# Kernel tuning notes

Measured on AMD Instinct MI355X. Metric: run time of the kernel, lower is better.

The kernel has to match this reference:

```python
import jax, jax.numpy as jnp
import numpy as np

B, S, D, H = 4, 2048, 1024, 16
DH = D // H


def setup_inputs() -> dict:
    key = jax.random.key(0)
    k0, k1, k2, k3 = jax.random.split(key, 4)
    x = jax.random.normal(k0, (B, S, D), dtype=jnp.float32)
    k = jax.random.normal(k1, (B, H, S, DH), dtype=jnp.float32)
    v = jax.random.normal(k2, (B, H, S, DH), dtype=jnp.float32)
    # nn.Linear(d, d, bias=False) weight: [out, in]; scaled like torch default init
    Wq = jax.random.normal(k3, (D, D), dtype=jnp.float32) * (1.0 / np.sqrt(D))
    return {"x": x, "k": k, "v": v, "Wq": Wq}


def reference(x, k, v, Wq):
    Bx, Sx, d = x.shape
    h, dh = k.shape[1], k.shape[3]
    rd = jnp.sqrt(jnp.float32(d))  # NOTE: module scales by sqrt(d), not sqrt(d_head)
    # q projection: y = x @ Wq.T  -> [B,S,d] -> [B,h,S,dh]
    q = (x @ Wq.T).reshape(Bx, Sx, h, dh).transpose(0, 2, 1, 3)
    # scores [B,h,S,S]
    a = jnp.einsum('bhqd,bhkd->bhqk', q, k) / rd
    causal = jnp.triu(jnp.ones((Sx, Sx), dtype=bool), k=1)
    a = jnp.where(causal, -jnp.inf, a)
    p = jax.nn.softmax(a, axis=-1)
    o = jnp.einsum('bhqk,bhkd->bhqd', p, v)  # [B,h,S,dh]
    o = o.transpose(0, 2, 1, 3).reshape(Bx, Sx, d)
    return x + o
```

## Files before the change

### kernel.cpp

```cpp
#include <hip/hip_runtime.h>
#include <hip/hip_bf16.h>

typedef __attribute__((ext_vector_type(4))) float f32x4;
typedef __attribute__((ext_vector_type(8))) short bf16x8;
typedef __attribute__((ext_vector_type(4))) unsigned short u16x4;

#define MFMA16(a, b, c) __builtin_amdgcn_mfma_f32_16x16x32_bf16((a), (b), (c), 0, 0, 0)

static __device__ __forceinline__ unsigned short f2bf(float f) {
    unsigned u = __float_as_uint(f);
    u += 0x7FFFu + ((u >> 16) & 1u);
    return (unsigned short)(u >> 16);
}
static __device__ __forceinline__ uint2 pack4_rhu(float4 v) {
    unsigned a = __float_as_uint(v.x) + 0x8000u;
    unsigned b = __float_as_uint(v.y) + 0x8000u;
    unsigned c = __float_as_uint(v.z) + 0x8000u;
    unsigned d = __float_as_uint(v.w) + 0x8000u;
    uint2 r;
    r.x = __builtin_amdgcn_perm(b, a, 0x07060302u);
    r.y = __builtin_amdgcn_perm(d, c, 0x07060302u);
    return r;
}
static __device__ __forceinline__ float exp2_fast(float x) {
#if __has_builtin(__builtin_amdgcn_exp2f)
    return __builtin_amdgcn_exp2f(x);
#else
    return exp2f(x);
#endif
}

#define QSCALE 0.04508422002778011f

__global__ __launch_bounds__(256) void qproj_kernel(const float* __restrict__ x,
                                                    const float* __restrict__ wq,
                                                    unsigned short* __restrict__ qout) {
    __shared__ __align__(16) unsigned short As[2][128][40];
    __shared__ __align__(16) unsigned short Bs[2][128][40];
    const int m0 = blockIdx.x * 128;
    const int n0 = blockIdx.y * 128;
    const int tid = threadIdx.x;
    const int wave = tid >> 6, lane = tid & 63;
    const int lg = lane >> 4, lc = lane & 15;
    const int wm = wave >> 1, wn = wave & 1;

    f32x4 acc[4][4];
#pragma unroll
    for (int i = 0; i < 4; ++i)
#pragma unroll
        for (int j = 0; j < 4; ++j) acc[i][j] = (f32x4){0.f, 0.f, 0.f, 0.f};

    float4 ax[4], bx[4];
#pragma unroll
    for (int i = 0; i < 4; ++i) {
        int c = tid + i * 256;
        int row = c >> 3, kc = (c & 7) * 4;
        ax[i] = *(const float4*)(x  + (size_t)(m0 + row) * 1024 + kc);
        bx[i] = *(const float4*)(wq + (size_t)(n0 + row) * 1024 + kc);
    }
#pragma unroll
    for (int i = 0; i < 4; ++i) {
        int c = tid + i * 256;
        int row = c >> 3, kc = (c & 7) * 4;
        *(uint2*)&As[0][row][kc] = pack4_rhu(ax[i]);
        *(uint2*)&Bs[0][row][kc] = pack4_rhu(bx[i]);
    }

    int cur = 0;
    for (int ki = 0; ki < 32; ++ki) {
        __syncthreads();
        const bool havenext = (ki + 1 < 32);
        if (havenext) {
            int ks = (ki + 1) * 32;
#pragma unroll
            for (int i = 0; i < 4; ++i) {
                int c = tid + i * 256;
                int row = c >> 3, kc = (c & 7) * 4;
                ax[i] = *(const float4*)(x  + (size_t)(m0 + row) * 1024 + ks + kc);
                bx[i] = *(const float4*)(wq + (size_t)(n0 + row) * 1024 + ks + kc);
            }
        }
        bf16x8 af[4], bfr[4];
#pragma unroll
        for (int i = 0; i < 4; ++i) {
            af[i]  = *(const bf16x8*)&As[cur][wm * 64 + i * 16 + lc][lg * 8];
            bfr[i] = *(const bf16x8*)&Bs[cur][wn * 64 + i * 16 + lc][lg * 8];
        }
        __builtin_amdgcn_s_setprio(1);
#pragma unroll
        for (int mi = 0; mi < 4; ++mi)
#pragma unroll
            for (int ni = 0; ni < 4; ++ni)
                acc[mi][ni] = MFMA16(af[mi], bfr[ni], acc[mi][ni]);
        __builtin_amdgcn_s_setprio(0);
        if (havenext) {
#pragma unroll
            for (int i = 0; i < 4; ++i) {
                int c = tid + i * 256;
                int row = c >> 3, kc = (c & 7) * 4;
                *(uint2*)&As[cur ^ 1][row][kc] = pack4_rhu(ax[i]);
                *(uint2*)&Bs[cur ^ 1][row][kc] = pack4_rhu(bx[i]);
            }
        }
        cur ^= 1;
    }
#pragma unroll
    for (int mi = 0; mi < 4; ++mi)
#pragma unroll
        for (int ni = 0; ni < 4; ++ni)
#pragma unroll
            for (int r = 0; r < 4; ++r) {
                int m = m0 + wm * 64 + mi * 16 + lg * 4 + r;
                int n = n0 + wn * 64 + ni * 16 + lc;
                int b = m >> 11, s = m & 2047;
                int h = n >> 6, dh = n & 63;
                qout[(((size_t)b * 16 + h) * 2048 + s) * 64 + dh] = f2bf(acc[mi][ni][r] * QSCALE);
            }
}

__global__ __launch_bounds__(256) void convtrans_kernel(const float* __restrict__ kin,
                                                        const float* __restrict__ vin,
                                                        unsigned short* __restrict__ kb,
                                                        unsigned short* __restrict__ vt) {
    __shared__ float buf[64][65];
    const int bid = blockIdx.x;
    const int tid = threadIdx.x;
    if (bid < 8192) {
        int i = bid * 256 + tid;
        float4 v = ((const float4*)kin)[i];
        u16x4 o = { f2bf(v.x), f2bf(v.y), f2bf(v.z), f2bf(v.w) };
        ((u16x4*)kb)[i] = o;
    } else {
        const int idx = bid - 8192;
        const int s0 = (idx & 31) * 64;
        const int bh = idx >> 5;
#pragma unroll
        for (int i = 0; i < 4; ++i) {
            int c = tid + i * 256;
            int s = c >> 4, dc = (c & 15) * 4;
            float4 val = *(const float4*)(vin + ((size_t)bh * 2048 + s0 + s) * 64 + dc);
            buf[s][dc] = val.x; buf[s][dc + 1] = val.y; buf[s][dc + 2] = val.z; buf[s][dc + 3] = val.w;
        }
        __syncthreads();
#pragma unroll
        for (int i = 0; i < 4; ++i) {
            int c = tid + i * 256;
            int dh = c >> 4, sc = (c & 15) * 4;
            u16x4 o = { f2bf(buf[sc][dh]), f2bf(buf[sc + 1][dh]), f2bf(buf[sc + 2][dh]), f2bf(buf[sc + 3][dh]) };
            *(u16x4*)(vt + ((size_t)bh * 64 + dh) * 2048 + s0 + sc) = o;
        }
    }
}

__global__ __launch_bounds__(256, 3) void attn_kernel(const unsigned short* __restrict__ qg,
                                                      const unsigned short* __restrict__ kg,
                                                      const unsigned short* __restrict__ vtg,
                                                      const float* __restrict__ x,
                                                      float* __restrict__ outp) {
    __shared__ __align__(16) unsigned short Ks[2][64][64];
    __shared__ __align__(16) unsigned short VTs[2][64][64];
    __shared__ __align__(16) unsigned short Ps[4][32][72];

    const int bh = blockIdx.x;
    const int qb = 15 - blockIdx.y;
    const int b = bh >> 4, h = bh & 15;
    const int tid = threadIdx.x;
    const int wave = tid >> 6, lane = tid & 63;
    const int lg = lane >> 4, lc = lane & 15;
    const int lc7 = lc & 7;
    const int qw0 = qb * 128 + wave * 32;
    const int nkv = 2 * qb + 2;

    const int r0  = tid >> 3;
    const int c16 = tid & 7;
    const int swz = (c16 ^ (r0 & 7)) * 8;
    const unsigned short* kbase = kg  + ((size_t)bh * 2048 + r0) * 64 + c16 * 8;
    const unsigned short* vbase = vtg + ((size_t)bh * 64 + r0) * 2048 + c16 * 8;

    bf16x8 qf[2][2];
#pragma unroll
    for (int qt = 0; qt < 2; ++qt)
#pragma unroll
        for (int c = 0; c < 2; ++c)
            qf[qt][c] = *(const bf16x8*)(qg + ((size_t)bh * 2048 + qw0 + qt * 16 + lc) * 64 + c * 32 + lg * 8);

    f32x4 oacc[2][4];
#pragma unroll
    for (int qt = 0; qt < 2; ++qt)
#pragma unroll
        for (int dt = 0; dt < 4; ++dt) oacc[qt][dt] = (f32x4){0.f, 0.f, 0.f, 0.f};
    float l_r[2] = {0.f, 0.f};

    {
        *(bf16x8*)&Ks[0][r0][swz]       = *(const bf16x8*)(kbase);
        *(bf16x8*)&Ks[0][r0 + 32][swz]  = *(const bf16x8*)(kbase + 2048);
        *(bf16x8*)&VTs[0][r0][swz]      = *(const bf16x8*)(vbase);
        *(bf16x8*)&VTs[0][r0 + 32][swz] = *(const bf16x8*)(vbase + 65536);
    }

    int cur = 0;
    for (int kv = 0; kv < nkv; ++kv) {
        __syncthreads();

        const bool havenext = (kv + 1 < nkv);
        const int nxt = havenext ? kv + 1 : kv;
        bf16x8 nk0 = *(const bf16x8*)(kbase + (size_t)nxt * 4096);
        bf16x8 nk1 = *(const bf16x8*)(kbase + (size_t)nxt * 4096 + 2048);
        bf16x8 nv0 = *(const bf16x8*)(vbase + nxt * 64);
        bf16x8 nv1 = *(const bf16x8*)(vbase + nxt * 64 + 65536);

        const bool active = (kv * 64 <= qw0 + 31);
        if (active) {
            bf16x8 kf[4][2];
#pragma unroll
            for (int kt = 0; kt < 4; ++kt)
#pragma unroll
                for (int c = 0; c < 2; ++c)
                    kf[kt][c] = *(const bf16x8*)&Ks[cur][kt * 16 + lc][((4 * c + lg) ^ lc7) * 8];

            const int kvb = kv * 64;
#pragma unroll
            for (int qt = 0; qt < 2; ++qt) {
                f32x4 st[4];
                __builtin_amdgcn_s_setprio(1);
#pragma unroll
                for (int kt = 0; kt < 4; ++kt) {
                    f32x4 a = (f32x4){0.f, 0.f, 0.f, 0.f};
                    a = MFMA16(kf[kt][0], qf[qt][0], a);
                    a = MFMA16(kf[kt][1], qf[qt][1], a);
                    st[kt] = a;
                }
                __builtin_amdgcn_s_setprio(0);

                float pp[4][4];
#pragma unroll
                for (int kt = 0; kt < 4; ++kt)
#pragma unroll
                    for (int r = 0; r < 4; ++r) pp[kt][r] = st[kt][r];
                if (kvb + 63 > qw0 + qt * 16) {
                    const int qrow = qw0 + qt * 16 + lc;
#pragma unroll
                    for (int kt = 0; kt < 4; ++kt)
#pragma unroll
                        for (int r = 0; r < 4; ++r) {
                            int kk = kvb + kt * 16 + lg * 4 + r;
                            if (kk > qrow) pp[kt][r] = -1e30f;
                        }
                }
                float rs = 0.f;
#pragma unroll
                for (int kt = 0; kt < 4; ++kt)
#pragma unroll
                    for (int r = 0; r < 4; ++r) {
                        float e = exp2_fast(pp[kt][r]);
                        pp[kt][r] = e;
                        rs += e;
                    }
                l_r[qt] += rs;
#pragma unroll
                for (int kt = 0; kt < 4; ++kt) {
                    uint2 w;
                    w.x = __builtin_amdgcn_perm(__float_as_uint(pp[kt][1]), __float_as_uint(pp[kt][0]), 0x07060302u);
                    w.y = __builtin_amdgcn_perm(__float_as_uint(pp[kt][3]), __float_as_uint(pp[kt][2]), 0x07060302u);
                    *(uint2*)&Ps[wave][qt * 16 + lc][kt * 16 + lg * 4] = w;
                }
            }
            asm volatile("s_waitcnt lgkmcnt(0)" ::: "memory");

            bf16x8 pf[2][2];
#pragma unroll
            for (int qt = 0; qt < 2; ++qt)
#pragma unroll
                for (int c = 0; c < 2; ++c)
                    pf[qt][c] = *(const bf16x8*)&Ps[wave][qt * 16 + lc][c * 32 + lg * 8];
            __builtin_amdgcn_s_setprio(1);
#pragma unroll
            for (int dt = 0; dt < 4; ++dt)
#pragma unroll
                for (int c = 0; c < 2; ++c) {
                    bf16x8 vtf = *(const bf16x8*)&VTs[cur][dt * 16 + lc][((4 * c + lg) ^ lc7) * 8];
#pragma unroll
                    for (int qt = 0; qt < 2; ++qt)
                        oacc[qt][dt] = MFMA16(vtf, pf[qt][c], oacc[qt][dt]);
                }
            __builtin_amdgcn_s_setprio(0);
        }

        if (havenext) {
            *(bf16x8*)&Ks[cur ^ 1][r0][swz]       = nk0;
            *(bf16x8*)&Ks[cur ^ 1][r0 + 32][swz]  = nk1;
            *(bf16x8*)&VTs[cur ^ 1][r0][swz]      = nv0;
            *(bf16x8*)&VTs[cur ^ 1][r0 + 32][swz] = nv1;
        }
        cur ^= 1;
    }

#pragma unroll
    for (int qt = 0; qt < 2; ++qt) {
        float lt = l_r[qt];
        lt += __shfl_xor(lt, 16, 64);
        lt += __shfl_xor(lt, 32, 64);
        float li = 1.0f / lt;
        const int q = qw0 + qt * 16 + lc;
        const size_t obase = ((size_t)b * 2048 + q) * 1024 + (size_t)h * 64 + lg * 4;
#pragma unroll
        for (int dt = 0; dt < 4; ++dt) {
            const size_t oi = obase + dt * 16;
            float4 xv = *(const float4*)(x + oi);
            float4 ov;
            ov.x = xv.x + oacc[qt][dt][0] * li;
            ov.y = xv.y + oacc[qt][dt][1] * li;
            ov.z = xv.z + oacc[qt][dt][2] * li;
            ov.w = xv.w + oacc[qt][dt][3] * li;
            *(float4*)(outp + oi) = ov;
        }
    }
}

extern "C" void kernel_launch(void* const* d_in, const int* in_sizes, int n_in,
                              void* d_out, int out_size, void* d_ws, size_t ws_size,
                              hipStream_t stream) {
    const float* x  = (const float*)d_in[0];
    const float* k  = (const float*)d_in[1];
    const float* v  = (const float*)d_in[2];
    const float* wq = (const float*)d_in[3];
    float* outp = (float*)d_out;

    const size_t NELEM = (size_t)4 * 2048 * 1024;
    unsigned short* qbuf = (unsigned short*)d_ws;
    unsigned short* kbuf = qbuf + NELEM;
    unsigned short* vtbuf = kbuf + NELEM;

    qproj_kernel<<<dim3(64, 8), 256, 0, stream>>>(x, wq, qbuf);
    convtrans_kernel<<<8192 + 2048, 256, 0, stream>>>(k, v, kbuf, vtbuf);
    attn_kernel<<<dim3(64, 16), 256, 0, stream>>>(qbuf, kbuf, vtbuf, x, outp);
}
```

Measured before the change: 98.70 us.

## Pair causal query blocks per workgroup and move P via permlane swaps

```diff
diff --git a/kernel.cpp b/kernel.cpp
--- a/kernel.cpp
+++ b/kernel.cpp
@@ -4,6 +4,7 @@
 typedef __attribute__((ext_vector_type(4))) float f32x4;
 typedef __attribute__((ext_vector_type(8))) short bf16x8;
 typedef __attribute__((ext_vector_type(4))) unsigned short u16x4;
+typedef __attribute__((ext_vector_type(4))) unsigned int u32x4;
 
 #define MFMA16(a, b, c) __builtin_amdgcn_mfma_f32_16x16x32_bf16((a), (b), (c), 0, 0, 0)
 
@@ -27,6 +28,25 @@
     return __builtin_amdgcn_exp2f(x);
 #else
     return exp2f(x);
+#endif
+}
+
+static __device__ __forceinline__ void permswap32(unsigned &a, unsigned &b) {
+#if __has_builtin(__builtin_amdgcn_permlane32_swap)
+    typedef __attribute__((ext_vector_type(2))) unsigned u32x2_t;
+    u32x2_t r = __builtin_amdgcn_permlane32_swap(a, b, false, false);
+    a = r[0]; b = r[1];
+#else
+    asm volatile("v_permlane32_swap_b32 %0, %1" : "+v"(a), "+v"(b));
+#endif
+}
+static __device__ __forceinline__ void permswap16(unsigned &a, unsigned &b) {
+#if __has_builtin(__builtin_amdgcn_permlane16_swap)
+    typedef __attribute__((ext_vector_type(2))) unsigned u32x2_t;
+    u32x2_t r = __builtin_amdgcn_permlane16_swap(a, b, false, false);
+    a = r[0]; b = r[1];
+#else
+    asm volatile("v_permlane16_swap_b32 %0, %1" : "+v"(a), "+v"(b));
 #endif
 }
 
@@ -152,24 +172,21 @@
     }
 }
 
-__global__ __launch_bounds__(256, 3) void attn_kernel(const unsigned short* __restrict__ qg,
-                                                      const unsigned short* __restrict__ kg,
-                                                      const unsigned short* __restrict__ vtg,
-                                                      const float* __restrict__ x,
-                                                      float* __restrict__ outp) {
+__global__ __launch_bounds__(256) void attn_kernel(const unsigned short* __restrict__ qg,
+                                                   const unsigned short* __restrict__ kg,
+                                                   const unsigned short* __restrict__ vtg,
+                                                   const float* __restrict__ x,
+                                                   float* __restrict__ outp) {
     __shared__ __align__(16) unsigned short Ks[2][64][64];
     __shared__ __align__(16) unsigned short VTs[2][64][64];
-    __shared__ __align__(16) unsigned short Ps[4][32][72];
 
     const int bh = blockIdx.x;
-    const int qb = 15 - blockIdx.y;
+    const int pr = blockIdx.y;
     const int b = bh >> 4, h = bh & 15;
     const int tid = threadIdx.x;
     const int wave = tid >> 6, lane = tid & 63;
     const int lg = lane >> 4, lc = lane & 15;
     const int lc7 = lc & 7;
-    const int qw0 = qb * 128 + wave * 32;
-    const int nkv = 2 * qb + 2;
 
     const int r0  = tid >> 3;
     const int c16 = tid & 7;
@@ -177,142 +194,159 @@
     const unsigned short* kbase = kg  + ((size_t)bh * 2048 + r0) * 64 + c16 * 8;
     const unsigned short* vbase = vtg + ((size_t)bh * 64 + r0) * 2048 + c16 * 8;
 
-    bf16x8 qf[2][2];
-#pragma unroll
-    for (int qt = 0; qt < 2; ++qt)
-#pragma unroll
-        for (int c = 0; c < 2; ++c)
-            qf[qt][c] = *(const bf16x8*)(qg + ((size_t)bh * 2048 + qw0 + qt * 16 + lc) * 64 + c * 32 + lg * 8);
-
-    f32x4 oacc[2][4];
-#pragma unroll
-    for (int qt = 0; qt < 2; ++qt)
-#pragma unroll
-        for (int dt = 0; dt < 4; ++dt) oacc[qt][dt] = (f32x4){0.f, 0.f, 0.f, 0.f};
-    float l_r[2] = {0.f, 0.f};
-
-    {
-        *(bf16x8*)&Ks[0][r0][swz]       = *(const bf16x8*)(kbase);
-        *(bf16x8*)&Ks[0][r0 + 32][swz]  = *(const bf16x8*)(kbase + 2048);
-        *(bf16x8*)&VTs[0][r0][swz]      = *(const bf16x8*)(vbase);
-        *(bf16x8*)&VTs[0][r0 + 32][swz] = *(const bf16x8*)(vbase + 65536);
-    }
-
     int cur = 0;
-    for (int kv = 0; kv < nkv; ++kv) {
-        __syncthreads();
-
-        const bool havenext = (kv + 1 < nkv);
-        const int nxt = havenext ? kv + 1 : kv;
-        bf16x8 nk0 = *(const bf16x8*)(kbase + (size_t)nxt * 4096);
-        bf16x8 nk1 = *(const bf16x8*)(kbase + (size_t)nxt * 4096 + 2048);
-        bf16x8 nv0 = *(const bf16x8*)(vbase + nxt * 64);
-        bf16x8 nv1 = *(const bf16x8*)(vbase + nxt * 64 + 65536);
-
-        const bool active = (kv * 64 <= qw0 + 31);
-        if (active) {
-            bf16x8 kf[4][2];
-#pragma unroll
-            for (int kt = 0; kt < 4; ++kt)
-#pragma unroll
-                for (int c = 0; c < 2; ++c)
-                    kf[kt][c] = *(const bf16x8*)&Ks[cur][kt * 16 + lc][((4 * c + lg) ^ lc7) * 8];
-
-            const int kvb = kv * 64;
-#pragma unroll
-            for (int qt = 0; qt < 2; ++qt) {
-                f32x4 st[4];
+    for (int seg = 0; seg < 2; ++seg) {
+        const int qb = seg ? (15 - pr) : pr;
+        const int qw0 = qb * 128 + wave * 32;
+        const int nkv = 2 * qb + 2;
+
+        bf16x8 qf[2][2];
+#pragma unroll
+        for (int qt = 0; qt < 2; ++qt)
+#pragma unroll
+            for (int c = 0; c < 2; ++c)
+                qf[qt][c] = *(const bf16x8*)(qg + ((size_t)bh * 2048 + qw0 + qt * 16 + lc) * 64 + c * 32 + lg * 8);
+
+        f32x4 oacc[2][4];
+#pragma unroll
+        for (int qt = 0; qt < 2; ++qt)
+#pragma unroll
+            for (int dt = 0; dt < 4; ++dt) oacc[qt][dt] = (f32x4){0.f, 0.f, 0.f, 0.f};
+        float l_r[2] = {0.f, 0.f};
+
+        {
+            *(bf16x8*)&Ks[cur][r0][swz]       = *(const bf16x8*)(kbase);
+            *(bf16x8*)&Ks[cur][r0 + 32][swz]  = *(const bf16x8*)(kbase + 2048);
+            *(bf16x8*)&VTs[cur][r0][swz]      = *(const bf16x8*)(vbase);
+            *(bf16x8*)&VTs[cur][r0 + 32][swz] = *(const bf16x8*)(vbase + 65536);
+        }
+
+        for (int kv = 0; kv < nkv; ++kv) {
+            __syncthreads();
+
+            const bool havenext = (kv + 1 < nkv);
+            const int nxt = havenext ? kv + 1 : kv;
+            bf16x8 nk0 = *(const bf16x8*)(kbase + (size_t)nxt * 4096);
+            bf16x8 nk1 = *(const bf16x8*)(kbase + (size_t)nxt * 4096 + 2048);
+            bf16x8 nv0 = *(const bf16x8*)(vbase + nxt * 64);
+            bf16x8 nv1 = *(const bf16x8*)(vbase + nxt * 64 + 65536);
+
+            const bool active = (kv * 64 <= qw0 + 31);
+            if (active) {
+                bf16x8 kf[4][2];
+#pragma unroll
+                for (int kt = 0; kt < 4; ++kt)
+#pragma unroll
+                    for (int c = 0; c < 2; ++c)
+                        kf[kt][c] = *(const bf16x8*)&Ks[cur][kt * 16 + lc][((4 * c + lg) ^ lc7) * 8];
+
+                const int kvb = kv * 64;
+                bf16x8 pf[2][2];
+#pragma unroll
+                for (int qt = 0; qt < 2; ++qt) {
+                    f32x4 st[4];
+                    __builtin_amdgcn_s_setprio(1);
+#pragma unroll
+                    for (int kt = 0; kt < 4; ++kt) {
+                        f32x4 a = (f32x4){0.f, 0.f, 0.f, 0.f};
+                        a = MFMA16(kf[kt][0], qf[qt][0], a);
+                        a = MFMA16(kf[kt][1], qf[qt][1], a);
+                        st[kt] = a;
+                    }
+                    __builtin_amdgcn_s_setprio(0);
+
+                    float pp[4][4];
+#pragma unroll
+                    for (int kt = 0; kt < 4; ++kt)
+#pragma unroll
+                        for (int r = 0; r < 4; ++r) pp[kt][r] = st[kt][r];
+                    if (kvb + 63 > qw0 + qt * 16) {
+                        const int qrow = qw0 + qt * 16 + lc;
+#pragma unroll
+                        for (int kt = 0; kt < 4; ++kt)
+#pragma unroll
+                            for (int r = 0; r < 4; ++r) {
+                                int kk = kvb + kt * 16 + lg * 4 + r;
+                                if (kk > qrow) pp[kt][r] = -1e30f;
+                            }
+                    }
+                    float rs = 0.f;
+#pragma unroll
+                    for (int kt = 0; kt < 4; ++kt)
+#pragma unroll
+                        for (int r = 0; r < 4; ++r) {
+                            float e = exp2_fast(pp[kt][r]);
+                            pp[kt][r] = e;
+                            rs += e;
+                        }
+                    l_r[qt] += rs;
+
+                    unsigned Wk[4][2];
+#pragma unroll
+                    for (int kt = 0; kt < 4; ++kt) {
+                        Wk[kt][0] = __builtin_amdgcn_perm(__float_as_uint(pp[kt][1]), __float_as_uint(pp[kt][0]), 0x07060302u);
+                        Wk[kt][1] = __builtin_amdgcn_perm(__float_as_uint(pp[kt][3]), __float_as_uint(pp[kt][2]), 0x07060302u);
+                    }
+                    unsigned T0[4], T1[4];
+#pragma unroll
+                    for (int hh = 0; hh < 2; ++hh) {
+                        unsigned a0 = Wk[0][hh], b0 = Wk[1][hh];
+                        permswap32(a0, b0);
+                        permswap16(a0, b0);
+                        T0[hh] = a0; T0[2 + hh] = b0;
+                        unsigned a1 = Wk[2][hh], b1 = Wk[3][hh];
+                        permswap32(a1, b1);
+                        permswap16(a1, b1);
+                        T1[hh] = a1; T1[2 + hh] = b1;
+                    }
+                    union { u32x4 u; bf16x8 v; } cv0, cv1;
+                    cv0.u = (u32x4){T0[0], T0[1], T0[2], T0[3]};
+                    cv1.u = (u32x4){T1[0], T1[1], T1[2], T1[3]};
+                    pf[qt][0] = cv0.v;
+                    pf[qt][1] = cv1.v;
+                }
+
                 __builtin_amdgcn_s_setprio(1);
 #pragma unroll
-                for (int kt = 0; kt < 4; ++kt) {
-                    f32x4 a = (f32x4){0.f, 0.f, 0.f, 0.f};
-                    a = MFMA16(kf[kt][0], qf[qt][0], a);
-                    a = MFMA16(kf[kt][1], qf[qt][1], a);
-                    st[kt] = a;
-                }
+                for (int dt = 0; dt < 4; ++dt)
+#pragma unroll
+                    for (int c = 0; c < 2; ++c) {
+                        bf16x8 vtf = *(const bf16x8*)&VTs[cur][dt * 16 + lc][((4 * c + lg) ^ lc7) * 8];
+#pragma unroll
+                        for (int qt = 0; qt < 2; ++qt)
+                            oacc[qt][dt] = MFMA16(vtf, pf[qt][c], oacc[qt][dt]);
+                    }
                 __builtin_amdgcn_s_setprio(0);
-
-                float pp[4][4];
-#pragma unroll
-                for (int kt = 0; kt < 4; ++kt)
-#pragma unroll
-                    for (int r = 0; r < 4; ++r) pp[kt][r] = st[kt][r];
-                if (kvb + 63 > qw0 + qt * 16) {
-                    const int qrow = qw0 + qt * 16 + lc;
-#pragma unroll
-                    for (int kt = 0; kt < 4; ++kt)
-#pragma unroll
-                        for (int r = 0; r < 4; ++r) {
-                            int kk = kvb + kt * 16 + lg * 4 + r;
-                            if (kk > qrow) pp[kt][r] = -1e30f;
-                        }
-                }
-                float rs = 0.f;
-#pragma unroll
-                for (int kt = 0; kt < 4; ++kt)
-#pragma unroll
-                    for (int r = 0; r < 4; ++r) {
-                        float e = exp2_fast(pp[kt][r]);
-                        pp[kt][r] = e;
-                        rs += e;
-                    }
-                l_r[qt] += rs;
-#pragma unroll
-                for (int kt = 0; kt < 4; ++kt) {
-                    uint2 w;
-                    w.x = __builtin_amdgcn_perm(__float_as_uint(pp[kt][1]), __float_as_uint(pp[kt][0]), 0x07060302u);
-                    w.y = __builtin_amdgcn_perm(__float_as_uint(pp[kt][3]), __float_as_uint(pp[kt][2]), 0x07060302u);
-                    *(uint2*)&Ps[wave][qt * 16 + lc][kt * 16 + lg * 4] = w;
-                }
-            }
-            asm volatile("s_waitcnt lgkmcnt(0)" ::: "memory");
-
-            bf16x8 pf[2][2];
-#pragma unroll
-            for (int qt = 0; qt < 2; ++qt)
-#pragma unroll
-                for (int c = 0; c < 2; ++c)
-                    pf[qt][c] = *(const bf16x8*)&Ps[wave][qt * 16 + lc][c * 32 + lg * 8];
-            __builtin_amdgcn_s_setprio(1);
-#pragma unroll
-            for (int dt = 0; dt < 4; ++dt)
-#pragma unroll
-                for (int c = 0; c < 2; ++c) {
-                    bf16x8 vtf = *(const bf16x8*)&VTs[cur][dt * 16 + lc][((4 * c + lg) ^ lc7) * 8];
-#pragma unroll
-                    for (int qt = 0; qt < 2; ++qt)
-                        oacc[qt][dt] = MFMA16(vtf, pf[qt][c], oacc[qt][dt]);
-                }
-            __builtin_amdgcn_s_setprio(0);
-        }
-
-        if (havenext) {
-            *(bf16x8*)&Ks[cur ^ 1][r0][swz]       = nk0;
-            *(bf16x8*)&Ks[cur ^ 1][r0 + 32][swz]  = nk1;
-            *(bf16x8*)&VTs[cur ^ 1][r0][swz]      = nv0;
-            *(bf16x8*)&VTs[cur ^ 1][r0 + 32][swz] = nv1;
-        }
-        cur ^= 1;
-    }
-
-#pragma unroll
-    for (int qt = 0; qt < 2; ++qt) {
-        float lt = l_r[qt];
-        lt += __shfl_xor(lt, 16, 64);
-        lt += __shfl_xor(lt, 32, 64);
-        float li = 1.0f / lt;
-        const int q = qw0 + qt * 16 + lc;
-        const size_t obase = ((size_t)b * 2048 + q) * 1024 + (size_t)h * 64 + lg * 4;
-#pragma unroll
-        for (int dt = 0; dt < 4; ++dt) {
-            const size_t oi = obase + dt * 16;
-            float4 xv = *(const float4*)(x + oi);
-            float4 ov;
-            ov.x = xv.x + oacc[qt][dt][0] * li;
-            ov.y = xv.y + oacc[qt][dt][1] * li;
-            ov.z = xv.z + oacc[qt][dt][2] * li;
-            ov.w = xv.w + oacc[qt][dt][3] * li;
-            *(float4*)(outp + oi) = ov;
+            }
+
+            if (havenext) {
+                *(bf16x8*)&Ks[cur ^ 1][r0][swz]       = nk0;
+                *(bf16x8*)&Ks[cur ^ 1][r0 + 32][swz]  = nk1;
+                *(bf16x8*)&VTs[cur ^ 1][r0][swz]      = nv0;
+                *(bf16x8*)&VTs[cur ^ 1][r0 + 32][swz] = nv1;
+            }
+            cur ^= 1;
+        }
+
+#pragma unroll
+        for (int qt = 0; qt < 2; ++qt) {
+            float lt = l_r[qt];
+            lt += __shfl_xor(lt, 16, 64);
+            lt += __shfl_xor(lt, 32, 64);
+            float li = 1.0f / lt;
+            const int q = qw0 + qt * 16 + lc;
+            const size_t obase = ((size_t)b * 2048 + q) * 1024 + (size_t)h * 64 + lg * 4;
+#pragma unroll
+            for (int dt = 0; dt < 4; ++dt) {
+                const size_t oi = obase + dt * 16;
+                float4 xv = *(const float4*)(x + oi);
+                float4 ov;
+                ov.x = xv.x + oacc[qt][dt][0] * li;
+                ov.y = xv.y + oacc[qt][dt][1] * li;
+                ov.z = xv.z + oacc[qt][dt][2] * li;
+                ov.w = xv.w + oacc[qt][dt][3] * li;
+                *(float4*)(outp + oi) = ov;
+            }
         }
     }
 }
@@ -333,5 +367,5 @@
 
     qproj_kernel<<<dim3(64, 8), 256, 0, stream>>>(x, wq, qbuf);
     convtrans_kernel<<<8192 + 2048, 256, 0, stream>>>(k, v, kbuf, vtbuf);
-    attn_kernel<<<dim3(64, 16), 256, 0, stream>>>(qbuf, kbuf, vtbuf, x, outp);
-}
+    attn_kernel<<<dim3(64, 8), 256, 0, stream>>>(qbuf, kbuf, vtbuf, x, outp);
+}
```

Measured after the change: 109.7 us. +11.1%, slower.
